# Performance work log

Hardware: AMD Instinct MI355X
Metric: run time of the kernel (lower is better)

## Reference

```python
import jax, jax.numpy as jnp
import numpy as np
from math import sqrt

NUM_HEADS = 8
HIDDEN = 768
ATTN_DIM = HIDDEN // NUM_HEADS  # 96
NEG = -1e10


def setup_inputs() -> dict:
    key = jax.random.key(0)
    ks = jax.random.split(key, 6)
    b, s, dim = 8, 1024, 768
    scale = 1.0 / sqrt(dim)
    return {
        "span_embeddings": jax.random.normal(ks[0], (b, s, dim), dtype=jnp.float32),
        "span_tags": jax.random.randint(ks[1], (b, s), 0, 5),
        "w_weight": jax.random.normal(ks[2], (1, dim), dtype=jnp.float32) * scale,
        "w_q": jax.random.normal(ks[3], (HIDDEN, dim), dtype=jnp.float32) * scale,
        "w_k": jax.random.normal(ks[4], (HIDDEN, dim), dtype=jnp.float32) * scale,
        "w_v": jax.random.normal(ks[5], (HIDDEN, dim), dtype=jnp.float32) * scale,
    }


def reference(span_embeddings, span_tags, w_weight, w_q, w_k, w_v):
    b, s, _ = span_embeddings.shape
    pad = span_tags == 0  # [b, s]

    # additive span attention weights: Linear(dim -> 1), mask padded, softmax over seq
    attn_weights = span_embeddings @ w_weight.T  # [b, s, 1]
    attn_weights = jnp.where(pad[:, :, None], NEG, attn_weights)
    attn_weights = jax.nn.softmax(attn_weights, axis=1)

    # NOTE: original views hidden as (attn_dim, num_heads) in that order
    qs = (span_embeddings @ w_q.T).reshape(b, s, ATTN_DIM, NUM_HEADS)
    ks = (span_embeddings @ w_k.T).reshape(b, s, ATTN_DIM, NUM_HEADS)
    vs = (span_embeddings @ w_v.T).reshape(b, s, ATTN_DIM, NUM_HEADS)

    rel = jnp.einsum('bqdh,bkdh->bqkh', qs, ks) / sqrt(ATTN_DIM)  # [b,q,k,h]
    # original masks along query axis (relevance_weights[span_tags.eq(0)] = NEG)
    rel = jnp.where(pad[:, :, None, None], NEG, rel)
    # original softmax(dim=-1) -> over the HEADS axis (faithful quirk)
    rel = jax.nn.softmax(rel, axis=-1)

    span_value = jnp.einsum('bqkh,bkdh->bqdh', rel, vs).reshape(b, s, HIDDEN)
    weighted_value = jnp.sum(attn_weights * span_value, axis=1)  # [b, hidden]
    return weighted_value
```

## Files before the change

kernel.cpp:

```cpp
#include <hip/hip_runtime.h>
#include <hip/hip_bf16.h>
#include <math.h>

#define NEGV (-1e10f)

typedef __attribute__((ext_vector_type(8))) short bf16x8;
typedef __attribute__((ext_vector_type(4))) float f32x4;
typedef __attribute__((ext_vector_type(16))) float f32x16;

static __device__ __forceinline__ unsigned short f2bf(float f) {
  unsigned int u = __builtin_bit_cast(unsigned int, f);
  unsigned int r = (u + 0x7fffu + ((u >> 16) & 1u)) >> 16;
  return (unsigned short)r;
}
static __device__ __forceinline__ float bf2f(unsigned short v) {
  return __builtin_bit_cast(float, (unsigned int)v << 16);
}
static __device__ __forceinline__ unsigned int pkbf(float lo, float hi) {
  unsigned int r;
  asm("v_cvt_pk_bf16_f32 %0, %1, %2" : "=v"(r) : "v"(lo), "v"(hi));
  return r;
}

#define GLD16(g, l)                                                   \
  __builtin_amdgcn_global_load_lds(                                   \
      (const __attribute__((address_space(1))) void*)(g),             \
      (__attribute__((address_space(3))) void*)(l), 16, 0, 0)

__global__ __launch_bounds__(256) void cast_inputs(
    const float* __restrict__ emb, const int* __restrict__ tags,
    const float* __restrict__ ww, const float* __restrict__ wq,
    const float* __restrict__ wk, const float* __restrict__ wv,
    unsigned short* __restrict__ embbf, float* __restrict__ logits,
    unsigned short* __restrict__ wbf) {
  int bx = blockIdx.x;
  if (bx < 2048) {
    int w = threadIdx.x >> 6, lane = threadIdx.x & 63;
    int row = bx * 4 + w;
    const float4* src = (const float4*)(emb + (size_t)row * 768);
    const float4* wsrc = (const float4*)ww;
    uint2* dst = (uint2*)(embbf + (size_t)row * 768);
    float d = 0.f;
#pragma unroll
    for (int j = 0; j < 3; j++) {
      int idx = lane + 64 * j;
      float4 v = src[idx];
      float4 wv = wsrc[idx];
      d += v.x * wv.x + v.y * wv.y + v.z * wv.z + v.w * wv.w;
      uint2 o;
      o.x = pkbf(v.x, v.y);
      o.y = pkbf(v.z, v.w);
      dst[idx] = o;
    }
#pragma unroll
    for (int off = 32; off; off >>= 1) d += __shfl_xor(d, off);
    if (lane == 0) logits[row] = (tags[row] == 0) ? NEGV : d;
  } else {
    int g = bx - 2048;
    int z = g / 576;
    int idx = (g - z * 576) * 256 + threadIdx.x;
    const float* src = (z == 0) ? wq : (z == 1) ? wk : wv;
    float4 v = ((const float4*)src)[idx];
    uint2 o;
    o.x = pkbf(v.x, v.y);
    o.y = pkbf(v.z, v.w);
    uint2* W2 = (uint2*)(wbf + (size_t)z * 589824);
    if (z == 2) {
      W2[idx] = o;
    } else {
      int f = idx / 192;
      int col4 = idx - f * 192;
      int h = f & 7, dg = f >> 3;
      int tt = dg >> 4, ddl = dg & 15;
      int wn = ddl >> 3, cb = (ddl >> 2) & 1, j = ddl & 3;
      int orow = tt * 128 + wn * 64 + j * 16 + cb * 8 + h;
      W2[orow * 192 + col4] = o;
    }
  }
}

__global__ __launch_bounds__(256) void softmax_aw(
    const float* __restrict__ logits, float* __restrict__ aw) {
  __shared__ float red[4];
  int b = blockIdx.x, t = threadIdx.x;
  const float* L = logits + b * 1024;
  float x0 = L[t], x1 = L[t + 256], x2 = L[t + 512], x3 = L[t + 768];
  float m = fmaxf(fmaxf(x0, x1), fmaxf(x2, x3));
#pragma unroll
  for (int off = 32; off; off >>= 1) m = fmaxf(m, __shfl_xor(m, off));
  if ((t & 63) == 0) red[t >> 6] = m;
  __syncthreads();
  m = fmaxf(fmaxf(red[0], red[1]), fmaxf(red[2], red[3]));
  float e0 = __expf(x0 - m), e1 = __expf(x1 - m), e2 = __expf(x2 - m),
        e3 = __expf(x3 - m);
  float s = e0 + e1 + e2 + e3;
#pragma unroll
  for (int off = 32; off; off >>= 1) s += __shfl_xor(s, off);
  __syncthreads();
  if ((t & 63) == 0) red[t >> 6] = s;
  __syncthreads();
  float inv = 1.0f / (red[0] + red[1] + red[2] + red[3]);
  float* A = aw + b * 1024;
  A[t] = e0 * inv; A[t + 256] = e1 * inv;
  A[t + 512] = e2 * inv; A[t + 768] = e3 * inv;
}

__global__ __launch_bounds__(256, 3) void qkv_gemm(
    const unsigned short* __restrict__ A, const unsigned short* __restrict__ Wbf,
    unsigned short* __restrict__ Qf, unsigned short* __restrict__ Kf,
    unsigned short* __restrict__ Vbf) {
  __shared__ __align__(16) unsigned short sm[24576];
  int g = blockIdx.x;
  int xcd = g & 7, local = g >> 3;
  int mbi = xcd * 8 + (local & 7);
  int nbz = local >> 3;
  int z = nbz / 6;
  int nbi = nbz - z * 6;
  const unsigned short* B = Wbf + (size_t)z * 589824;
  int mb = mbi * 128, nb = nbi * 128;
  int tid = threadIdx.x;
  int w = tid >> 6, lane = tid & 63;
  int wm = w >> 1, wn = w & 1;
  int c = lane & 15, quad = lane >> 4;
  int lrow = lane >> 2;
  int lcol = ((lane & 3) ^ ((lrow >> 1) & 3)) * 8;
  const unsigned short* Ag = A + (size_t)(mb + w * 32 + lrow) * 768 + lcol;
  const unsigned short* Bg = B + (size_t)(nb + w * 32 + lrow) * 768 + lcol;
  int woff = w * 1024;

#define PREFETCH(buf, kb)                                                   \
  do {                                                                      \
    GLD16(Ag + (kb), sm + (buf) * 8192 + woff);                             \
    GLD16(Ag + (kb) + 16 * 768, sm + (buf) * 8192 + woff + 512);            \
    GLD16(Bg + (kb), sm + (buf) * 8192 + 4096 + woff);                      \
    GLD16(Bg + (kb) + 16 * 768, sm + (buf) * 8192 + 4096 + woff + 512);     \
  } while (0)

  f32x4 acc[4][4];
#pragma unroll
  for (int i = 0; i < 4; i++)
#pragma unroll
    for (int j = 0; j < 4; j++) acc[i][j] = 0;

  PREFETCH(0, 0);
  PREFETCH(1, 32);

  int rd = 0;
  int sw = (quad ^ ((c >> 1) & 3)) * 8;
  for (int it = 0; it < 24; it++) {
    if (it < 23) {
      asm volatile("s_waitcnt vmcnt(4) lgkmcnt(0)" ::: "memory");
    } else {
      asm volatile("s_waitcnt vmcnt(0) lgkmcnt(0)" ::: "memory");
    }
    __builtin_amdgcn_s_barrier();
    if (it + 2 < 24) {
      int wr = rd + 2;
      if (wr >= 3) wr -= 3;
      PREFETCH(wr, (it + 2) * 32);
    }
    const unsigned short* Ab = sm + rd * 8192;
    const unsigned short* Bb = Ab + 4096;
    bf16x8 af[4], bfr[4];
#pragma unroll
    for (int i = 0; i < 4; i++)
      af[i] = *(const bf16x8*)&Ab[(wm * 64 + i * 16 + c) * 32 + sw];
#pragma unroll
    for (int j = 0; j < 4; j++)
      bfr[j] = *(const bf16x8*)&Bb[(wn * 64 + j * 16 + c) * 32 + sw];
#pragma unroll
    for (int i = 0; i < 4; i++)
#pragma unroll
      for (int j = 0; j < 4; j++)
        acc[i][j] = __builtin_amdgcn_mfma_f32_16x16x32_bf16(af[i], bfr[j],
                                                            acc[i][j], 0, 0, 0);
    rd = (rd == 2) ? 0 : rd + 1;
  }
  __syncthreads();

  if (z == 2) {
#pragma unroll
    for (int i = 0; i < 4; i++)
#pragma unroll
      for (int j = 0; j < 4; j++)
#pragma unroll
        for (int r = 0; r < 4; r++) {
          int rl = wm * 64 + i * 16 + quad * 4 + r;
          int cl = wn * 64 + j * 16 + c;
          sm[rl * 136 + cl] = f2bf(acc[i][j][r]);
        }
    __syncthreads();
#pragma unroll
    for (int it2 = 0; it2 < 8; it2++) {
      int g2 = it2 * 256 + tid;
      int rl = g2 >> 4;
      int cu = (g2 & 15) * 8;
      bf16x8 vdat = *(const bf16x8*)&sm[rl * 136 + cu];
      *(bf16x8*)&Vbf[(size_t)(mb + rl) * 768 + nb + cu] = vdat;
    }
  } else {
    unsigned short* O = (z == 0) ? Qf : Kf;
#pragma unroll
    for (int i = 0; i < 4; i++) {
#pragma unroll
      for (int r = 0; r < 4; r++) {
        int qlr = wm * 64 + i * 16 + quad * 4 + r;
        int chunkL = (qlr >> 5) * 8 + (c & 7);
        int lane32 = (qlr & 31) + wn * 32;
        uint2 o;
        o.x = pkbf(acc[i][0][r], acc[i][1][r]);
        o.y = pkbf(acc[i][2][r], acc[i][3][r]);
        *(uint2*)&sm[chunkL * 520 + lane32 * 8 + 4 * (c >> 3)] = o;
      }
    }
    __syncthreads();
    int bq = mb >> 10;
    int qt32g0 = (mb & 1023) >> 5;
    int tt = nbi;
#pragma unroll
    for (int it2 = 0; it2 < 8; it2++) {
      int gg = it2 * 256 + tid;
      int chunkL = gg >> 6;
      int off = (gg & 63) * 8;
      bf16x8 vdat = *(const bf16x8*)&sm[chunkL * 520 + off];
      int qt32 = qt32g0 + (chunkL >> 3), h = chunkL & 7;
      size_t dst = ((((size_t)(bq * 32 + qt32) * 8 + h) * 6 + tt) << 9) + off;
      *(bf16x8*)&O[dst] = vdat;
    }
  }
#undef PREFETCH
}

__global__ __launch_bounds__(256) void attn(
    const unsigned short* __restrict__ Qf, const unsigned short* __restrict__ Kf,
    const float* __restrict__ aw, float* __restrict__ Ptp) {
  __shared__ float pbuf[1024];
  int id = blockIdx.x;
  int b = id & 7, qb = (id >> 3) & 15, kb = id >> 7;
  int tid = threadIdx.x, w = tid >> 6, lane = tid & 63;
  int wq = w >> 1, wk = w & 1;
  const unsigned short* Qb =
      Qf + ((size_t)(b * 32 + qb * 2 + wq) * 48) * 512 + (size_t)lane * 8;
  const unsigned short* Kb =
      Kf + ((size_t)(b * 32 + kb * 2 + wk) * 48) * 512 + (size_t)lane * 8;

  f32x16 acc[8];
#pragma unroll
  for (int h = 0; h < 8; h++) acc[h] = 0;
#pragma unroll
  for (int h = 0; h < 8; h++) {
#pragma unroll
    for (int t = 0; t < 6; t++) {
      bf16x8 a = *(const bf16x8*)(Qb + (size_t)(h * 6 + t) * 512);
      bf16x8 bb = *(const bf16x8*)(Kb + (size_t)(h * 6 + t) * 512);
      acc[h] = __builtin_amdgcn_mfma_f32_32x32x16_bf16(a, bb, acc[h], 0, 0, 0);
    }
  }

  float awv[16];
#pragma unroll
  for (int reg = 0; reg < 16; reg++) {
    int row = (reg & 3) + 8 * (reg >> 2) + 4 * (lane >> 5);
    awv[reg] = aw[b * 1024 + qb * 64 + wq * 32 + row];
  }
  float partial[8];
#pragma unroll
  for (int h = 0; h < 8; h++) partial[h] = 0.f;
  const float C2 = 0.10206207261596577f * 1.4426950408889634f;
#pragma unroll
  for (int reg = 0; reg < 16; reg++) {
    float v[8];
    float ssum = 0.f;
#pragma unroll
    for (int h = 0; h < 8; h++) {
      float e = exp2f(acc[h][reg] * C2);
      v[h] = e;
      ssum += e;
    }
    float g = awv[reg] * __builtin_amdgcn_rcpf(ssum);
#pragma unroll
    for (int h = 0; h < 8; h++) partial[h] += v[h] * g;
  }
#pragma unroll
  for (int h = 0; h < 8; h++) {
    float v = partial[h];
    v += __shfl_xor(v, 32);
    partial[h] = v;
  }
  if (lane < 32) {
#pragma unroll
    for (int h = 0; h < 8; h++) pbuf[w * 256 + lane * 8 + h] = partial[h];
  }
  __syncthreads();
#pragma unroll
  for (int wk2 = 0; wk2 < 2; wk2++) {
    float s = pbuf[wk2 * 256 + tid] + pbuf[(2 + wk2) * 256 + tid];
    int kcol = tid >> 3, h = tid & 7;
    Ptp[(((size_t)qb * 8 + b) * 1024 + kb * 64 + wk2 * 32 + kcol) * 8 + h] = s;
  }
}

__global__ __launch_bounds__(256) void finalize(
    const float* __restrict__ Ptp, const unsigned short* __restrict__ Vbf,
    float* __restrict__ out) {
  __shared__ float ps[256];
  int kc = blockIdx.x, b = blockIdx.y;
  int t = threadIdx.x;
  {
    int k = kc * 32 + (t >> 3), h = t & 7;
    float s = 0.f;
#pragma unroll
    for (int qc = 0; qc < 16; qc++)
      s += Ptp[(((size_t)qc * 8 + b) * 1024 + k) * 8 + h];
    ps[t] = s;
  }
  __syncthreads();
  if (t < 192) {
    int o0 = t * 4;
    int hb = o0 & 7;
    float a0 = 0, a1 = 0, a2 = 0, a3 = 0;
    const unsigned short* Vb = Vbf + ((size_t)b * 1024 + kc * 32) * 768 + o0;
#pragma unroll 4
    for (int kk = 0; kk < 32; kk++) {
      ushort4 vv = *(const ushort4*)(Vb + (size_t)kk * 768);
      const float* p = &ps[kk * 8 + hb];
      a0 += p[0] * bf2f(vv.x);
      a1 += p[1] * bf2f(vv.y);
      a2 += p[2] * bf2f(vv.z);
      a3 += p[3] * bf2f(vv.w);
    }
    atomicAdd(&out[b * 768 + o0], a0);
    atomicAdd(&out[b * 768 + o0 + 1], a1);
    atomicAdd(&out[b * 768 + o0 + 2], a2);
    atomicAdd(&out[b * 768 + o0 + 3], a3);
  }
}

extern "C" void kernel_launch(void* const* d_in, const int* in_sizes, int n_in,
                              void* d_out, int out_size, void* d_ws,
                              size_t ws_size, hipStream_t stream) {
  const float* emb = (const float*)d_in[0];
  const int* tags = (const int*)d_in[1];
  const float* ww = (const float*)d_in[2];
  const float* wq = (const float*)d_in[3];
  const float* wk = (const float*)d_in[4];
  const float* wv = (const float*)d_in[5];
  float* out = (float*)d_out;
  char* ws = (char*)d_ws;
  unsigned short* embbf = (unsigned short*)(ws + 0);
  unsigned short* wbf   = (unsigned short*)(ws + 12582912);
  unsigned short* Qf    = (unsigned short*)(ws + 16121856);
  unsigned short* Kf    = (unsigned short*)(ws + 28704768);
  unsigned short* Vbf   = (unsigned short*)(ws + 41287680);
  float* logits         = (float*)(ws + 53870592);
  float* aw             = (float*)(ws + 53903360);
  float* Ptp            = (float*)(ws + 53936128);

  hipMemsetAsync(out, 0, 8 * 768 * sizeof(float), stream);
  cast_inputs<<<3776, 256, 0, stream>>>(emb, tags, ww, wq, wk, wv, embbf,
                                        logits, wbf);
  softmax_aw<<<8, 256, 0, stream>>>(logits, aw);
  qkv_gemm<<<1152, 256, 0, stream>>>(embbf, wbf, Qf, Kf, Vbf);
  attn<<<2048, 256, 0, stream>>>(Qf, Kf, aw, Ptp);
  finalize<<<dim3(32, 8), 256, 0, stream>>>(Ptp, Vbf, out);
}
```

Measured before the change: 161.5 us.

## Fuse span softmax into attn, fold score scale into Wq, drop memset

Removes the separate softmax_aw launch and the hipMemsetAsync. Each attn block now recomputes the per-batch softmax over 1024 logits into shared memory, and cast_inputs zeroes the output in its last block. The 1/sqrt(d)*log2e scale is folded into the bf16 Wq so the attn epilogue skips a multiply per score, and the first head's Q/K loads are issued before the softmax to hide latency. The cost is redundant softmax work in all 2048 attn blocks, extra barriers, and slightly different bf16 rounding of the scaled Wq.

```diff
diff --git a/kernel.cpp b/kernel.cpp
--- a/kernel.cpp
+++ b/kernel.cpp
@@ -32,7 +32,7 @@
     const float* __restrict__ ww, const float* __restrict__ wq,
     const float* __restrict__ wk, const float* __restrict__ wv,
     unsigned short* __restrict__ embbf, float* __restrict__ logits,
-    unsigned short* __restrict__ wbf) {
+    unsigned short* __restrict__ wbf, float* __restrict__ out) {
   int bx = blockIdx.x;
   if (bx < 2048) {
     int w = threadIdx.x >> 6, lane = threadIdx.x & 63;
@@ -61,6 +61,10 @@
     int idx = (g - z * 576) * 256 + threadIdx.x;
     const float* src = (z == 0) ? wq : (z == 1) ? wk : wv;
     float4 v = ((const float4*)src)[idx];
+    if (z == 0) {
+      const float C2 = 0.10206207261596577f * 1.4426950408889634f;
+      v.x *= C2; v.y *= C2; v.z *= C2; v.w *= C2;
+    }
     uint2 o;
     o.x = pkbf(v.x, v.y);
     o.y = pkbf(v.z, v.w);
@@ -76,33 +80,12 @@
       int orow = tt * 128 + wn * 64 + j * 16 + cb * 8 + h;
       W2[orow * 192 + col4] = o;
     }
-  }
-}
-
-__global__ __launch_bounds__(256) void softmax_aw(
-    const float* __restrict__ logits, float* __restrict__ aw) {
-  __shared__ float red[4];
-  int b = blockIdx.x, t = threadIdx.x;
-  const float* L = logits + b * 1024;
-  float x0 = L[t], x1 = L[t + 256], x2 = L[t + 512], x3 = L[t + 768];
-  float m = fmaxf(fmaxf(x0, x1), fmaxf(x2, x3));
-#pragma unroll
-  for (int off = 32; off; off >>= 1) m = fmaxf(m, __shfl_xor(m, off));
-  if ((t & 63) == 0) red[t >> 6] = m;
-  __syncthreads();
-  m = fmaxf(fmaxf(red[0], red[1]), fmaxf(red[2], red[3]));
-  float e0 = __expf(x0 - m), e1 = __expf(x1 - m), e2 = __expf(x2 - m),
-        e3 = __expf(x3 - m);
-  float s = e0 + e1 + e2 + e3;
-#pragma unroll
-  for (int off = 32; off; off >>= 1) s += __shfl_xor(s, off);
-  __syncthreads();
-  if ((t & 63) == 0) red[t >> 6] = s;
-  __syncthreads();
-  float inv = 1.0f / (red[0] + red[1] + red[2] + red[3]);
-  float* A = aw + b * 1024;
-  A[t] = e0 * inv; A[t + 256] = e1 * inv;
-  A[t + 512] = e2 * inv; A[t + 768] = e3 * inv;
+    if (bx == 3775) {
+      float4 z4 = {0.f, 0.f, 0.f, 0.f};
+#pragma unroll
+      for (int q = 0; q < 6; q++) ((float4*)out)[q * 256 + threadIdx.x] = z4;
+    }
+  }
 }
 
 __global__ __launch_bounds__(256, 3) void qkv_gemm(
@@ -233,8 +216,9 @@
 
 __global__ __launch_bounds__(256) void attn(
     const unsigned short* __restrict__ Qf, const unsigned short* __restrict__ Kf,
-    const float* __restrict__ aw, float* __restrict__ Ptp) {
+    const float* __restrict__ logits, float* __restrict__ Ptp) {
   __shared__ float pbuf[1024];
+  __shared__ float red[4];
   int id = blockIdx.x;
   int b = id & 7, qb = (id >> 3) & 15, kb = id >> 7;
   int tid = threadIdx.x, w = tid >> 6, lane = tid & 63;
@@ -244,6 +228,38 @@
   const unsigned short* Kb =
       Kf + ((size_t)(b * 32 + kb * 2 + wk) * 48) * 512 + (size_t)lane * 8;
 
+  bf16x8 qa[6], ka[6];
+#pragma unroll
+  for (int t = 0; t < 6; t++) {
+    qa[t] = *(const bf16x8*)(Qb + (size_t)t * 512);
+    ka[t] = *(const bf16x8*)(Kb + (size_t)t * 512);
+  }
+
+  {
+    const float* L = logits + b * 1024;
+    float x0 = L[tid], x1 = L[tid + 256], x2 = L[tid + 512], x3 = L[tid + 768];
+    float m = fmaxf(fmaxf(x0, x1), fmaxf(x2, x3));
+#pragma unroll
+    for (int off = 32; off; off >>= 1) m = fmaxf(m, __shfl_xor(m, off));
+    if ((tid & 63) == 0) red[tid >> 6] = m;
+    __syncthreads();
+    m = fmaxf(fmaxf(red[0], red[1]), fmaxf(red[2], red[3]));
+    float e0 = __expf(x0 - m), e1 = __expf(x1 - m), e2 = __expf(x2 - m),
+          e3 = __expf(x3 - m);
+    float s = e0 + e1 + e2 + e3;
+#pragma unroll
+    for (int off = 32; off; off >>= 1) s += __shfl_xor(s, off);
+    __syncthreads();
+    if ((tid & 63) == 0) red[tid >> 6] = s;
+    __syncthreads();
+    float inv = 1.0f / (red[0] + red[1] + red[2] + red[3]);
+    pbuf[tid] = e0 * inv;
+    pbuf[tid + 256] = e1 * inv;
+    pbuf[tid + 512] = e2 * inv;
+    pbuf[tid + 768] = e3 * inv;
+    __syncthreads();
+  }
+
   f32x16 acc[8];
 #pragma unroll
   for (int h = 0; h < 8; h++) acc[h] = 0;
@@ -251,8 +267,8 @@
   for (int h = 0; h < 8; h++) {
 #pragma unroll
     for (int t = 0; t < 6; t++) {
-      bf16x8 a = *(const bf16x8*)(Qb + (size_t)(h * 6 + t) * 512);
-      bf16x8 bb = *(const bf16x8*)(Kb + (size_t)(h * 6 + t) * 512);
+      bf16x8 a = (h == 0) ? qa[t] : *(const bf16x8*)(Qb + (size_t)(h * 6 + t) * 512);
+      bf16x8 bb = (h == 0) ? ka[t] : *(const bf16x8*)(Kb + (size_t)(h * 6 + t) * 512);
       acc[h] = __builtin_amdgcn_mfma_f32_32x32x16_bf16(a, bb, acc[h], 0, 0, 0);
     }
   }
@@ -261,19 +277,19 @@
 #pragma unroll
   for (int reg = 0; reg < 16; reg++) {
     int row = (reg & 3) + 8 * (reg >> 2) + 4 * (lane >> 5);
-    awv[reg] = aw[b * 1024 + qb * 64 + wq * 32 + row];
-  }
+    awv[reg] = pbuf[qb * 64 + wq * 32 + row];
+  }
+  __syncthreads();
   float partial[8];
 #pragma unroll
   for (int h = 0; h < 8; h++) partial[h] = 0.f;
-  const float C2 = 0.10206207261596577f * 1.4426950408889634f;
 #pragma unroll
   for (int reg = 0; reg < 16; reg++) {
     float v[8];
     float ssum = 0.f;
 #pragma unroll
     for (int h = 0; h < 8; h++) {
-      float e = exp2f(acc[h][reg] * C2);
+      float e = exp2f(acc[h][reg]);
       v[h] = e;
       ssum += e;
     }
@@ -353,14 +369,11 @@
   unsigned short* Kf    = (unsigned short*)(ws + 28704768);
   unsigned short* Vbf   = (unsigned short*)(ws + 41287680);
   float* logits         = (float*)(ws + 53870592);
-  float* aw             = (float*)(ws + 53903360);
   float* Ptp            = (float*)(ws + 53936128);
 
-  hipMemsetAsync(out, 0, 8 * 768 * sizeof(float), stream);
   cast_inputs<<<3776, 256, 0, stream>>>(emb, tags, ww, wq, wk, wv, embbf,
-                                        logits, wbf);
-  softmax_aw<<<8, 256, 0, stream>>>(logits, aw);
+                                        logits, wbf, out);
   qkv_gemm<<<1152, 256, 0, stream>>>(embbf, wbf, Qf, Kf, Vbf);
-  attn<<<2048, 256, 0, stream>>>(Qf, Kf, aw, Ptp);
+  attn<<<2048, 256, 0, stream>>>(Qf, Kf, logits, Ptp);
   finalize<<<dim3(32, 8), 256, 0, stream>>>(Ptp, Vbf, out);
 }
```

After: 159.7 us, median of 2. About the same (-1.1%).
